# Optimization experiments

Measured on AMD Instinct MI355X. Metric: run time of the kernel, lower is better.

The kernel has to match this reference:

```python
import jax, jax.numpy as jnp
import numpy as np

B_GRAPHS = 32   # number of graphs in the batch (static)
HEADS = 8
EPS = 1e-8


def _layer_norm(x, g, b):
    mu = x.mean(-1, keepdims=True)
    var = x.var(-1, keepdims=True)
    return (x - mu) * jax.lax.rsqrt(var + 1e-5) * g + b


def setup_inputs() -> dict:
    key = jax.random.key(0)
    ks = jax.random.split(key, 16)
    N, C, d, M = 5120, 128, 16, 256
    E = N * 16
    f32 = jnp.float32
    sc_c = 1.0 / np.sqrt(C)
    inp = {
        'x': jax.random.normal(ks[0], (N, C), f32),
        'pe_re': jax.random.normal(ks[1], (N, d), f32),
        'pe_im': jax.random.normal(ks[2], (N, d), f32),
        'wq': jax.random.normal(ks[3], (C, C), f32) * sc_c,
        'bq': jnp.zeros((C,), f32),
        'wk': jax.random.normal(ks[4], (C, C), f32) * sc_c,
        'bk': jnp.zeros((C,), f32),
        'wv': jax.random.normal(ks[5], (C, C), f32) * sc_c,
        'bv': jnp.zeros((C,), f32),
        'wo': jax.random.normal(ks[6], (C, C), f32) * sc_c,
        'bo': jnp.zeros((C,), f32),
        'pe_w1': jax.random.normal(ks[7], (4 * d, 2 * d), f32) * (1.0 / np.sqrt(4 * d)),
        'pe_b1': jnp.zeros((2 * d,), f32),
        'pe_w2': jax.random.normal(ks[8], (2 * d, HEADS), f32) * (1.0 / np.sqrt(2 * d)),
        'pe_b2': jnp.zeros((HEADS,), f32),
        'mlp_w1': jax.random.normal(ks[9], (C, 2 * C), f32) * sc_c,
        'mlp_b1': jnp.zeros((2 * C,), f32),
        'mlp_w2': jax.random.normal(ks[10], (2 * C, C), f32) * (1.0 / np.sqrt(2 * C)),
        'mlp_b2': jnp.zeros((C,), f32),
        'ln2_g': jnp.ones((C,), f32),
        'ln2_b': jnp.zeros((C,), f32),
        'ln3_g': jnp.ones((C,), f32),
        'ln3_b': jnp.zeros((C,), f32),
        'batch': jnp.sort(jax.random.randint(ks[11], (N,), 0, B_GRAPHS, jnp.int32)),
        'edge_index': jax.random.randint(ks[12], (2, E), 0, N, jnp.int32),
        'nmax': M,
    }
    return inp


def reference(x, pe_re, pe_im, wq, bq, wk, bk, wv, bv, wo, bo,
              pe_w1, pe_b1, pe_w2, pe_b2, mlp_w1, mlp_b1, mlp_w2, mlp_b2,
              ln2_g, ln2_b, ln3_g, ln3_b, batch, edge_index, nmax):
    N, C = x.shape
    H = HEADS
    dh = C // H
    M = nmax

    # --- to_dense_batch: ragged [N,*] -> dense [B, M, *] + mask ---
    counts = jax.ops.segment_sum(jnp.ones((N,), jnp.int32), batch, num_segments=B_GRAPHS)
    offsets = jnp.concatenate([jnp.zeros((1,), jnp.int32), jnp.cumsum(counts)[:-1]])
    intra = jnp.arange(N, dtype=jnp.int32) - offsets[batch]
    hd = jnp.zeros((B_GRAPHS, M, C), x.dtype).at[batch, intra].set(x)
    ar = jnp.zeros((B_GRAPHS, M, pe_re.shape[1]), x.dtype).at[batch, intra].set(pe_re)
    ai = jnp.zeros((B_GRAPHS, M, pe_im.shape[1]), x.dtype).at[batch, intra].set(pe_im)
    mask = jnp.zeros((B_GRAPHS, M), bool).at[batch, intra].set(True)

    # --- pairwise complex-angle PE bias ---
    pn = jnp.sqrt(ar * ar + ai * ai + EPS)                 # [B,M,d] complex_norm
    denom = pn[:, :, None, :] * pn[:, None, :, :] + EPS    # [B,M,M,d]
    # z_i * conj(z_j) normalized -> cos/sin of pairwise angle
    real = (ar[:, :, None, :] * ar[:, None, :, :] + ai[:, :, None, :] * ai[:, None, :, :]) / denom
    imag = (ai[:, :, None, :] * ar[:, None, :, :] - ar[:, :, None, :] * ai[:, None, :, :]) / denom
    pni = jnp.broadcast_to(pn[:, :, None, :], real.shape)
    pnj = jnp.broadcast_to(pn[:, None, :, :], real.shape)
    bias_in = jnp.concatenate([pni, pnj, real, imag], axis=-1)       # [B,M,M,4d]
    hb = jax.nn.relu(bias_in @ pe_w1 + pe_b1) @ pe_w2 + pe_b2        # [B,M,M,H]
    # torch: bias.transpose(1,-1) swaps dims 1 and 3 -> [B,H,M,M]
    bias = jnp.transpose(hb, (0, 3, 2, 1))                           # [B,H,q,k]

    # --- multi-head attention with float bias + key padding mask ---
    q = (hd @ wq + bq).reshape(B_GRAPHS, M, H, dh)
    k = (hd @ wk + bk).reshape(B_GRAPHS, M, H, dh)
    v = (hd @ wv + bv).reshape(B_GRAPHS, M, H, dh)
    scores = jnp.einsum('bihd,bjhd->bhij', q, k) / np.sqrt(dh) + bias
    scores = jnp.where(mask[:, None, None, :], scores, -1e9)
    attn = jax.nn.softmax(scores, axis=-1)
    o = jnp.einsum('bhij,bjhd->bihd', attn, v).reshape(B_GRAPHS, M, C)
    o = o @ wo + bo

    # --- back to ragged, residual, norms, FFN ---
    h = o[batch, intra] + x
    h = _layer_norm(h, ln2_g, ln2_b)
    out = h + (jax.nn.relu(h @ mlp_w1 + mlp_b1) @ mlp_w2 + mlp_b2)
    out = _layer_norm(out, ln3_g, ln3_b)
    return out
```

## Files before the change

kernel.cpp:

```cpp
#include <hip/hip_runtime.h>

#define N_NODES 5120
#define C_DIM   128
#define D_PE    16
#define M_MAX   256
#define B_G     32
#define H_HEADS 8
#define DH      16
#define EPS_PE  1e-8f
#define QT      4
#define SCP     264

#define WS_COUNTS   0
#define WS_OFFSETS  32
#define WS_INTRA    64
#define WS_MASK     5184
#define WS_HD       13376
#define WS_AR       1061952
#define WS_AI       1193024
#define WS_PN       1324096
#define WS_CN       1455168
#define WS_KFHI     1717312
#define WS_KFLO     1979456
#define WS_Q        2110528
#define WS_K        3159104
#define WS_V        4207680
#define WS_OATT     5256256
#define WS_OPROJ    6304832
#define WS_HLN      7353408
#define WS_FFNH     8008768
#define WS_FFNO     9319488
#define WS_BIAS     9974848
#define WS_WPK_HI   18363456
#define WS_WPK_LO   18428992
#define WS_ZERO_FLOATS 1324096

#define WOFF_Q   0
#define WOFF_K   16384
#define WOFF_V   32768
#define WOFF_O   49152
#define WOFF_W1  65536
#define WOFF_W2  98304

typedef __attribute__((ext_vector_type(8))) short bf8_t;
typedef __attribute__((ext_vector_type(4))) float f4_t;

__device__ inline short f2bf(float f) {
    union { float f; unsigned u; } v; v.f = f;
    unsigned r = (v.u + 0x7FFF + ((v.u >> 16) & 1)) >> 16;
    return (short)r;
}
__device__ inline float bf2f(short h) {
    union { unsigned u; float f; } v; v.u = ((unsigned)(unsigned short)h) << 16;
    return v.f;
}
__device__ inline unsigned pack2(short a, short b) {
    return (unsigned)(unsigned short)a | ((unsigned)(unsigned short)b << 16);
}
__device__ inline bf8_t bf8_from2(uint2 a, uint2 b) {
    bf8_t o;
    o[0]=(short)a.x; o[1]=(short)(a.x>>16); o[2]=(short)a.y; o[3]=(short)(a.y>>16);
    o[4]=(short)b.x; o[5]=(short)(b.x>>16); o[6]=(short)b.y; o[7]=(short)(b.y>>16);
    return o;
}

__global__ __launch_bounds__(256) void setup_kernel(
    const int* __restrict__ batch, int* __restrict__ offsets, int* __restrict__ intra)
{
    __shared__ int cnt[B_G];
    __shared__ int off[B_G];
    const int t = threadIdx.x;
    if (t < B_G) cnt[t] = 0;
    __syncthreads();
    for (int n = t; n < N_NODES; n += 256) atomicAdd(&cnt[batch[n]], 1);
    __syncthreads();
    if (t == 0) { int s = 0; for (int b = 0; b < B_G; ++b) { off[b] = s; s += cnt[b]; } }
    __syncthreads();
    if (t < B_G) offsets[t] = off[t];
    for (int n = t; n < N_NODES; n += 256) intra[n] = n - off[batch[n]];
}

__global__ __launch_bounds__(128) void scatter_kernel(
    const float* __restrict__ x, const float* __restrict__ pre, const float* __restrict__ pim,
    const int* __restrict__ batch, const int* __restrict__ intra,
    float* __restrict__ hd, float* __restrict__ ar, float* __restrict__ ai,
    int* __restrict__ mask)
{
    const int n = blockIdx.x, c = threadIdx.x;
    const int b = batch[n], m = intra[n];
    hd[((size_t)b * M_MAX + m) * C_DIM + c] = x[(size_t)n * C_DIM + c];
    if (c < D_PE) {
        ar[((size_t)b * M_MAX + m) * D_PE + c] = pre[(size_t)n * D_PE + c];
        ai[((size_t)b * M_MAX + m) * D_PE + c] = pim[(size_t)n * D_PE + c];
    }
    if (c == 0) mask[b * M_MAX + m] = 1;
}

__global__ __launch_bounds__(256) void prep_kernel(
    const float* __restrict__ ar, const float* __restrict__ ai,
    float* __restrict__ pn, float* __restrict__ cn,
    unsigned short* __restrict__ kf_hi, unsigned short* __restrict__ kf_lo)
{
    const int idx = blockIdx.x * 256 + threadIdx.x;
    const int cell = idx >> 4, dd = idx & 15;
    const float a = ar[idx], b = ai[idx];
    const float p = sqrtf(a * a + b * b + EPS_PE);
    const float inv = 1.f / p;
    const float cr = a * inv, ci = b * inv;
    pn[idx] = p;
    cn[(size_t)cell * 32 + dd]      = cr;
    cn[(size_t)cell * 32 + 16 + dd] = ci;
    const size_t hb = (size_t)cell * 64, lb = (size_t)cell * 32;
    short crh = f2bf(cr), cih = f2bf(ci);
    kf_hi[hb + dd]      = (unsigned short)crh;
    kf_hi[hb + 16 + dd] = (unsigned short)cih;
    kf_hi[hb + 32 + dd] = (unsigned short)f2bf(p);
    kf_hi[hb + 48 + dd] = (dd == 0) ? (unsigned short)f2bf(1.f) : 0;
    kf_lo[lb + dd]      = (unsigned short)f2bf(cr - bf2f(crh));
    kf_lo[lb + 16 + dd] = (unsigned short)f2bf(ci - bf2f(cih));
}

__global__ __launch_bounds__(256) void wpack_kernel(
    const float* __restrict__ wq, const float* __restrict__ wk,
    const float* __restrict__ wv, const float* __restrict__ wo,
    const float* __restrict__ w1, const float* __restrict__ w2,
    unsigned short* __restrict__ hi, unsigned short* __restrict__ lo)
{
    const int tid = blockIdx.x * 256 + threadIdx.x;
    const int tile = tid >> 6, lane = tid & 63;
    const float* W; int N, ltile; size_t off;
    if (tile < 128) {
        const int wi = tile >> 5; ltile = tile & 31; N = 128;
        W = (wi == 0) ? wq : (wi == 1) ? wk : (wi == 2) ? wv : wo;
        off = (size_t)wi * 16384;
    } else if (tile < 192) { ltile = tile - 128; N = 256; W = w1; off = WOFF_W1; }
    else                   { ltile = tile - 192; N = 128; W = w2; off = WOFF_W2; }
    const int NT = N / 16;
    const int kt = ltile / NT, nt = ltile % NT;
    const int col = nt * 16 + (lane & 15);
    const int k0  = kt * 32 + (lane >> 4) * 8;
    bf8_t vhi, vlo;
    #pragma unroll
    for (int e = 0; e < 8; ++e) {
        const float v = W[(size_t)(k0 + e) * N + col];
        const short h = f2bf(v);
        vhi[e] = h; vlo[e] = f2bf(v - bf2f(h));
    }
    const size_t toff = off + ((size_t)ltile * 64 + lane) * 8;
    *(bf8_t*)(hi + toff) = vhi;
    *(bf8_t*)(lo + toff) = vlo;
}

template<int K, int N, bool RELU, bool RES>
__device__ inline void mgemm_body(
    const float* __restrict__ A, const unsigned short* __restrict__ hi,
    const unsigned short* __restrict__ lo,
    const float* __restrict__ bias, const float* __restrict__ res,
    float* __restrict__ out, int bx)
{
    constexpr int NT = N / 16, KT = K / 32;
    const int rb = bx * 64;
    const int w = threadIdx.x >> 6, lane = threadIdx.x & 63;
    const int arow = rb + w * 16 + (lane & 15);
    const int g = lane >> 4;

    f4_t acc[NT];
    #pragma unroll
    for (int nt = 0; nt < NT; ++nt) acc[nt] = (f4_t){0.f, 0.f, 0.f, 0.f};

    #pragma unroll
    for (int kt = 0; kt < KT; ++kt) {
        const float* ap = A + (size_t)arow * K + kt * 32 + g * 8;
        const float4 a0 = *(const float4*)ap;
        const float4 a1 = *(const float4*)(ap + 4);
        const float av[8] = {a0.x, a0.y, a0.z, a0.w, a1.x, a1.y, a1.z, a1.w};
        bf8_t ahi, alo;
        #pragma unroll
        for (int e = 0; e < 8; ++e) {
            const short h = f2bf(av[e]);
            ahi[e] = h; alo[e] = f2bf(av[e] - bf2f(h));
        }
        #pragma unroll
        for (int nt = 0; nt < NT; ++nt) {
            const size_t toff = ((size_t)(kt * NT + nt) * 64 + lane) * 8;
            const bf8_t bhi = *(const bf8_t*)(hi + toff);
            const bf8_t blo = *(const bf8_t*)(lo + toff);
            acc[nt] = __builtin_amdgcn_mfma_f32_16x16x32_bf16(ahi, bhi, acc[nt], 0, 0, 0);
            acc[nt] = __builtin_amdgcn_mfma_f32_16x16x32_bf16(alo, bhi, acc[nt], 0, 0, 0);
            acc[nt] = __builtin_amdgcn_mfma_f32_16x16x32_bf16(ahi, blo, acc[nt], 0, 0, 0);
        }
    }

    const int orow0 = rb + w * 16 + g * 4;
    #pragma unroll
    for (int nt = 0; nt < NT; ++nt) {
        const int col = nt * 16 + (lane & 15);
        const float bv = bias[col];
        #pragma unroll
        for (int r = 0; r < 4; ++r) {
            float v = acc[nt][r] + bv;
            if (RELU) v = fmaxf(v, 0.f);
            if (RES)  v += res[(size_t)(orow0 + r) * N + col];
            out[(size_t)(orow0 + r) * N + col] = v;
        }
    }
}

__global__ __launch_bounds__(256) void qkv_kernel(
    const float* __restrict__ A,
    const unsigned short* __restrict__ hi, const unsigned short* __restrict__ lo,
    const float* __restrict__ bq, const float* __restrict__ bk, const float* __restrict__ bv,
    float* __restrict__ qm, float* __restrict__ km, float* __restrict__ vm)
{
    const int sel = blockIdx.y;
    const float* bias = (sel == 0) ? bq : (sel == 1) ? bk : bv;
    float* out = (sel == 0) ? qm : (sel == 1) ? km : vm;
    const size_t woff = (size_t)sel * 16384;
    mgemm_body<128, 128, false, false>(A, hi + woff, lo + woff, bias, nullptr, out, blockIdx.x);
}

template<int K, int N, bool RELU, bool RES>
__global__ __launch_bounds__(256) void mgemm_kernel(
    const float* __restrict__ A,
    const unsigned short* __restrict__ hi, const unsigned short* __restrict__ lo,
    const float* __restrict__ bias, const float* __restrict__ res, float* __restrict__ out)
{
    mgemm_body<K, N, RELU, RES>(A, hi, lo, bias, res, out, blockIdx.x);
}

__global__ __launch_bounds__(512) void bias_kernel(
    const float* __restrict__ cn, const float* __restrict__ pn,
    const unsigned short* __restrict__ kf_hi, const unsigned short* __restrict__ kf_lo,
    const float* __restrict__ w1, const float* __restrict__ b1,
    const float* __restrict__ w2, const float* __restrict__ b2,
    unsigned short* __restrict__ bias_out)
{
    __shared__ float sW1T[32][65];
    __shared__ float s_cn[16][32];
    __shared__ float s_pn[16][16];
    __shared__ uint2 s_scr[8][16][10];

    const int b  = blockIdx.y;
    const int i0 = blockIdx.x * 16;
    const int t  = threadIdx.x;

    for (int idx = t; idx < 2048; idx += 512) {
        int f = idx >> 5, hh = idx & 31;
        sW1T[hh][f] = w1[f * 32 + hh];
    }
    { int il = t >> 5, c = t & 31;
      s_cn[il][c] = cn[((size_t)(b * 256 + i0 + il)) * 32 + c]; }
    if (t < 256) { int il = t >> 4, dd = t & 15;
      s_pn[il][dd] = pn[((size_t)(b * 256 + i0 + il)) * 16 + dd]; }
    __syncthreads();

    const int w    = t >> 6;
    const int lane = t & 63;
    const int lj   = lane & 15;
    const int g    = lane >> 4;

    bf8_t a2f;
    #pragma unroll
    for (int e = 0; e < 8; ++e) {
        float v = (lj < 8) ? w2[(g * 8 + e) * 8 + lj] : 0.f;
        a2f[e] = f2bf(v);
    }
    float b2v0 = 0.f, b2v1 = 0.f, b2v2 = 0.f, b2v3 = 0.f;
    if (g < 2) { b2v0 = b2[g*4+0]; b2v1 = b2[g*4+1]; b2v2 = b2[g*4+2]; b2v3 = b2[g*4+3]; }

    for (int ii = 0; ii < 2; ++ii) {
        const int il = w * 2 + ii;
        const int i  = i0 + il;

        float vrow0 = b1[lj], vrow1 = b1[16 + lj];
        #pragma unroll
        for (int dd = 0; dd < 16; ++dd) {
            float p = s_pn[il][dd];
            vrow0 = fmaf(sW1T[lj][16 + dd],      p, vrow0);
            vrow1 = fmaf(sW1T[16 + lj][16 + dd], p, vrow1);
        }

        bf8_t a0hi0, a0lo0, a1f0, a0hi1, a0lo1, a1f1;
        #pragma unroll
        for (int e = 0; e < 8; ++e) {
            const int dd = (g & 1) * 8 + e;
            const float cr = s_cn[il][dd], ci = s_cn[il][16 + dd];
            {
                float wr = sW1T[lj][32 + dd], wi = sW1T[lj][48 + dd];
                float val = (g < 2) ? (wr * cr - wi * ci) : (wr * ci + wi * cr);
                short hi = f2bf(val);
                a0hi0[e] = hi; a0lo0[e] = f2bf(val - bf2f(hi));
                float v1 = (g < 2) ? sW1T[lj][g * 8 + e]
                                   : ((g == 2 && e == 0) ? vrow0 : 0.f);
                a1f0[e] = f2bf(v1);
            }
            {
                float wr = sW1T[16 + lj][32 + dd], wi = sW1T[16 + lj][48 + dd];
                float val = (g < 2) ? (wr * cr - wi * ci) : (wr * ci + wi * cr);
                short hi = f2bf(val);
                a0hi1[e] = hi; a0lo1[e] = f2bf(val - bf2f(hi));
                float v1 = (g < 2) ? sW1T[16 + lj][g * 8 + e]
                                   : ((g == 2 && e == 0) ? vrow1 : 0.f);
                a1f1[e] = f2bf(v1);
            }
        }

        for (int jt = 0; jt < 16; ++jt) {
            const size_t node = (size_t)b * 256 + jt * 16 + lj;
            const bf8_t* ph = (const bf8_t*)(kf_hi + node * 64);
            const bf8_t* pl = (const bf8_t*)(kf_lo + node * 32);
            bf8_t b0hi = ph[g];
            bf8_t b0lo = pl[g];
            bf8_t b1f  = ph[4 + g];

            f4_t acc0 = {0.f, 0.f, 0.f, 0.f}, acc1 = {0.f, 0.f, 0.f, 0.f};
            acc0 = __builtin_amdgcn_mfma_f32_16x16x32_bf16(a0hi0, b0hi, acc0, 0, 0, 0);
            acc0 = __builtin_amdgcn_mfma_f32_16x16x32_bf16(a0hi0, b0lo, acc0, 0, 0, 0);
            acc0 = __builtin_amdgcn_mfma_f32_16x16x32_bf16(a0lo0, b0hi, acc0, 0, 0, 0);
            acc0 = __builtin_amdgcn_mfma_f32_16x16x32_bf16(a1f0,  b1f,  acc0, 0, 0, 0);
            acc1 = __builtin_amdgcn_mfma_f32_16x16x32_bf16(a0hi1, b0hi, acc1, 0, 0, 0);
            acc1 = __builtin_amdgcn_mfma_f32_16x16x32_bf16(a0hi1, b0lo, acc1, 0, 0, 0);
            acc1 = __builtin_amdgcn_mfma_f32_16x16x32_bf16(a0lo1, b0hi, acc1, 0, 0, 0);
            acc1 = __builtin_amdgcn_mfma_f32_16x16x32_bf16(a1f1,  b1f,  acc1, 0, 0, 0);

            uint2 w0, w1p;
            w0.x  = pack2(f2bf(fmaxf(acc0[0], 0.f)), f2bf(fmaxf(acc0[1], 0.f)));
            w0.y  = pack2(f2bf(fmaxf(acc0[2], 0.f)), f2bf(fmaxf(acc0[3], 0.f)));
            w1p.x = pack2(f2bf(fmaxf(acc1[0], 0.f)), f2bf(fmaxf(acc1[1], 0.f)));
            w1p.y = pack2(f2bf(fmaxf(acc1[2], 0.f)), f2bf(fmaxf(acc1[3], 0.f)));
            s_scr[w][lj][g]     = w0;
            s_scr[w][lj][4 + g] = w1p;
            __builtin_amdgcn_s_waitcnt(0);

            uint2 q0 = s_scr[w][lj][2 * g];
            uint2 q1 = s_scr[w][lj][2 * g + 1];
            bf8_t hb = bf8_from2(q0, q1);

            f4_t acc2 = {0.f, 0.f, 0.f, 0.f};
            acc2 = __builtin_amdgcn_mfma_f32_16x16x32_bf16(a2f, hb, acc2, 0, 0, 0);

            if (g < 2) {
                uint2 st;
                st.x = pack2(f2bf(acc2[0] + b2v0), f2bf(acc2[1] + b2v1));
                st.y = pack2(f2bf(acc2[2] + b2v2), f2bf(acc2[3] + b2v3));
                size_t idx = (((size_t)b * 256 + i) * 256 + jt * 16 + lj) * 8 + g * 4;
                *(uint2*)(bias_out + idx) = st;
            }
        }
    }
}

__global__ __launch_bounds__(256) void attn_kernel(
    const float* __restrict__ qm, const float* __restrict__ km, const float* __restrict__ vm,
    const int* __restrict__ mask, const unsigned short* __restrict__ bias,
    float* __restrict__ o_att)
{
    const int b  = blockIdx.y;
    const int i0 = blockIdx.x * QT;
    const int t  = threadIdx.x;
    const int j  = t;

    __shared__ float s_q[QT][C_DIM];
    __shared__ float s_sc[QT][H_HEADS][SCP];

    for (int idx = t; idx < QT * C_DIM; idx += 256) {
        const int qi = idx >> 7, c = idx & 127;
        s_q[qi][c] = qm[((size_t)(b * 256 + i0 + qi)) * C_DIM + c];
    }
    __syncthreads();

    const int mj = mask[b * M_MAX + j];
    uint4 bu[QT];
    #pragma unroll
    for (int qi = 0; qi < QT; ++qi)
        bu[qi] = *(const uint4*)(bias + (((size_t)(b * 256 + i0 + qi)) * 256 + j) * 8);

    const float* krow = km + ((size_t)(b * 256 + j)) * C_DIM;
    #pragma unroll
    for (int h = 0; h < 8; ++h) {
        float kv[DH];
        #pragma unroll
        for (int q4 = 0; q4 < 4; ++q4) {
            float4 v = ((const float4*)(krow + h * DH))[q4];
            kv[q4*4+0]=v.x; kv[q4*4+1]=v.y; kv[q4*4+2]=v.z; kv[q4*4+3]=v.w;
        }
        #pragma unroll
        for (int qi = 0; qi < QT; ++qi) {
            float dot = 0.f;
            #pragma unroll
            for (int dd = 0; dd < DH; ++dd)
                dot = fmaf(s_q[qi][h * DH + dd], kv[dd], dot);
            const unsigned u = ((const unsigned*)&bu[qi])[h >> 1];
            const float bv = bf2f((short)((h & 1) ? (u >> 16) : (u & 0xffff)));
            s_sc[qi][h][j] = mj ? fmaf(dot, 0.25f, bv) : -1e9f;
        }
    }
    __syncthreads();

    {
        const int wave = t >> 6, lane = t & 63;
        for (int r = wave; r < QT * H_HEADS; r += 4) {
            float* row = ((float*)s_sc) + r * SCP;
            float x0 = row[lane], x1 = row[lane + 64], x2 = row[lane + 128], x3 = row[lane + 192];
            float mx = fmaxf(fmaxf(x0, x1), fmaxf(x2, x3));
            #pragma unroll
            for (int off = 32; off > 0; off >>= 1) mx = fmaxf(mx, __shfl_xor(mx, off, 64));
            float e0 = expf(x0 - mx), e1 = expf(x1 - mx), e2 = expf(x2 - mx), e3 = expf(x3 - mx);
            float s = e0 + e1 + e2 + e3;
            #pragma unroll
            for (int off = 32; off > 0; off >>= 1) s += __shfl_xor(s, off, 64);
            const float inv = 1.f / s;
            row[lane] = e0 * inv; row[lane + 64] = e1 * inv;
            row[lane + 128] = e2 * inv; row[lane + 192] = e3 * inv;
        }
    }
    __syncthreads();

    {
        const int c = t & 127;
        const int gq = t >> 7;
        const int h = c >> 4;
        const int qA = gq * 2, qB = gq * 2 + 1;
        const float* vb = vm + (size_t)b * M_MAX * C_DIM + c;
        float a0 = 0.f, a1 = 0.f;
        for (int jj = 0; jj < M_MAX; jj += 4) {
            float4 pA = *(const float4*)&s_sc[qA][h][jj];
            float4 pB = *(const float4*)&s_sc[qB][h][jj];
            float v0 = vb[(size_t)(jj + 0) * C_DIM];
            float v1 = vb[(size_t)(jj + 1) * C_DIM];
            float v2 = vb[(size_t)(jj + 2) * C_DIM];
            float v3 = vb[(size_t)(jj + 3) * C_DIM];
            a0 = fmaf(pA.x, v0, a0); a0 = fmaf(pA.y, v1, a0);
            a0 = fmaf(pA.z, v2, a0); a0 = fmaf(pA.w, v3, a0);
            a1 = fmaf(pB.x, v0, a1); a1 = fmaf(pB.y, v1, a1);
            a1 = fmaf(pB.z, v2, a1); a1 = fmaf(pB.w, v3, a1);
        }
        o_att[((size_t)(b * 256 + i0 + qA)) * C_DIM + c] = a0;
        o_att[((size_t)(b * 256 + i0 + qB)) * C_DIM + c] = a1;
    }
}

__global__ __launch_bounds__(128) void gather_res_ln_kernel(
    const float* __restrict__ op, const float* __restrict__ x,
    const int* __restrict__ batch, const int* __restrict__ intra,
    const float* __restrict__ g, const float* __restrict__ be, float* __restrict__ out)
{
    const int n = blockIdx.x, c = threadIdx.x;
    const int b = batch[n], m = intra[n];
    const float v = op[((size_t)b * M_MAX + m) * C_DIM + c] + x[(size_t)n * C_DIM + c];
    float s = v, sq = v * v;
    #pragma unroll
    for (int off = 32; off > 0; off >>= 1) {
        s  += __shfl_xor(s, off, 64);
        sq += __shfl_xor(sq, off, 64);
    }
    __shared__ float red[4];
    if ((threadIdx.x & 63) == 0) {
        red[(threadIdx.x >> 6) * 2]     = s;
        red[(threadIdx.x >> 6) * 2 + 1] = sq;
    }
    __syncthreads();
    s = red[0] + red[2]; sq = red[1] + red[3];
    const float mu  = s * (1.f / C_DIM);
    const float var = sq * (1.f / C_DIM) - mu * mu;
    const float sc  = rsqrtf(var + 1e-5f);
    out[(size_t)n * C_DIM + c] = (v - mu) * sc * g[c] + be[c];
}

__global__ __launch_bounds__(128) void ln_kernel(
    const float* __restrict__ in, const float* __restrict__ g,
    const float* __restrict__ be, float* __restrict__ out)
{
    const int n = blockIdx.x, c = threadIdx.x;
    const float v = in[(size_t)n * C_DIM + c];
    float s = v, sq = v * v;
    #pragma unroll
    for (int off = 32; off > 0; off >>= 1) {
        s  += __shfl_xor(s, off, 64);
        sq += __shfl_xor(sq, off, 64);
    }
    __shared__ float red[4];
    if ((threadIdx.x & 63) == 0) {
        red[(threadIdx.x >> 6) * 2]     = s;
        red[(threadIdx.x >> 6) * 2 + 1] = sq;
    }
    __syncthreads();
    s = red[0] + red[2]; sq = red[1] + red[3];
    const float mu  = s * (1.f / C_DIM);
    const float var = sq * (1.f / C_DIM) - mu * mu;
    const float sc  = rsqrtf(var + 1e-5f);
    out[(size_t)n * C_DIM + c] = (v - mu) * sc * g[c] + be[c];
}

extern "C" void kernel_launch(void* const* d_in, const int* in_sizes, int n_in,
                              void* d_out, int out_size, void* d_ws, size_t ws_size,
                              hipStream_t stream)
{
    const float* x      = (const float*)d_in[0];
    const float* pe_re  = (const float*)d_in[1];
    const float* pe_im  = (const float*)d_in[2];
    const float* wq     = (const float*)d_in[3];
    const float* bq     = (const float*)d_in[4];
    const float* wk     = (const float*)d_in[5];
    const float* bk     = (const float*)d_in[6];
    const float* wv     = (const float*)d_in[7];
    const float* bv     = (const float*)d_in[8];
    const float* wo     = (const float*)d_in[9];
    const float* bo     = (const float*)d_in[10];
    const float* pe_w1  = (const float*)d_in[11];
    const float* pe_b1  = (const float*)d_in[12];
    const float* pe_w2  = (const float*)d_in[13];
    const float* pe_b2  = (const float*)d_in[14];
    const float* mlp_w1 = (const float*)d_in[15];
    const float* mlp_b1 = (const float*)d_in[16];
    const float* mlp_w2 = (const float*)d_in[17];
    const float* mlp_b2 = (const float*)d_in[18];
    const float* ln2_g  = (const float*)d_in[19];
    const float* ln2_b  = (const float*)d_in[20];
    const float* ln3_g  = (const float*)d_in[21];
    const float* ln3_b  = (const float*)d_in[22];
    const int*   batch  = (const int*)d_in[23];

    float* ws = (float*)d_ws;
    int*   offsets = (int*)(ws + WS_OFFSETS);
    int*   intra   = (int*)(ws + WS_INTRA);
    int*   mask    = (int*)(ws + WS_MASK);
    float* hd   = ws + WS_HD;
    float* ar   = ws + WS_AR;
    float* ai   = ws + WS_AI;
    float* pn   = ws + WS_PN;
    float* cn   = ws + WS_CN;
    unsigned short* kf_hi = (unsigned short*)(ws + WS_KFHI);
    unsigned short* kf_lo = (unsigned short*)(ws + WS_KFLO);
    float* qm   = ws + WS_Q;
    float* km   = ws + WS_K;
    float* vm   = ws + WS_V;
    float* oatt = ws + WS_OATT;
    float* oprj = ws + WS_OPROJ;
    float* hln  = ws + WS_HLN;
    float* ffnh = ws + WS_FFNH;
    float* ffno = ws + WS_FFNO;
    unsigned short* bias = (unsigned short*)(ws + WS_BIAS);
    unsigned short* wpk_hi = (unsigned short*)(ws + WS_WPK_HI);
    unsigned short* wpk_lo = (unsigned short*)(ws + WS_WPK_LO);
    float* outp = (float*)d_out;

    hipMemsetAsync(d_ws, 0, (size_t)WS_ZERO_FLOATS * sizeof(float), stream);

    setup_kernel<<<1, 256, 0, stream>>>(batch, offsets, intra);
    wpack_kernel<<<64, 256, 0, stream>>>(wq, wk, wv, wo, mlp_w1, mlp_w2, wpk_hi, wpk_lo);
    scatter_kernel<<<N_NODES, 128, 0, stream>>>(x, pe_re, pe_im, batch, intra, hd, ar, ai, mask);
    prep_kernel<<<512, 256, 0, stream>>>(ar, ai, pn, cn, kf_hi, kf_lo);

    qkv_kernel<<<dim3(128, 3), 256, 0, stream>>>(hd, wpk_hi, wpk_lo, bq, bk, bv, qm, km, vm);

    bias_kernel<<<dim3(16, 32), 512, 0, stream>>>(cn, pn, kf_hi, kf_lo,
                                                  pe_w1, pe_b1, pe_w2, pe_b2, bias);

    attn_kernel<<<dim3(M_MAX / QT, B_G), 256, 0, stream>>>(qm, km, vm, mask, bias, oatt);

    mgemm_kernel<128, 128, false, false><<<128, 256, 0, stream>>>(
        oatt, wpk_hi + WOFF_O, wpk_lo + WOFF_O, bo, nullptr, oprj);
    gather_res_ln_kernel<<<N_NODES, 128, 0, stream>>>(oprj, x, batch, intra, ln2_g, ln2_b, hln);
    mgemm_kernel<128, 256, true, false><<<80, 256, 0, stream>>>(
        hln, wpk_hi + WOFF_W1, wpk_lo + WOFF_W1, mlp_b1, nullptr, ffnh);
    mgemm_kernel<256, 128, false, true><<<80, 256, 0, stream>>>(
        ffnh, wpk_hi + WOFF_W2, wpk_lo + WOFF_W2, mlp_b2, hln, ffno);
    ln_kernel<<<N_NODES, 128, 0, stream>>>(ffno, ln3_g, ln3_b, outp);
}
```

Before: 315.1 us.

## Fuse scatter into QKV/prep, fuse GEMM with residual+LayerNorm, skip padded rows

Result: slower. 325.1 us (+3.2%).

```diff
diff --git a/kernel.cpp b/kernel.cpp
--- a/kernel.cpp
+++ b/kernel.cpp
@@ -8,36 +8,28 @@
 #define H_HEADS 8
 #define DH      16
 #define EPS_PE  1e-8f
-#define QT      4
+#define QT      2
 #define SCP     264
 
 #define WS_COUNTS   0
 #define WS_OFFSETS  32
 #define WS_INTRA    64
 #define WS_MASK     5184
-#define WS_HD       13376
-#define WS_AR       1061952
-#define WS_AI       1193024
-#define WS_PN       1324096
-#define WS_CN       1455168
-#define WS_KFHI     1717312
-#define WS_KFLO     1979456
-#define WS_Q        2110528
-#define WS_K        3159104
-#define WS_V        4207680
-#define WS_OATT     5256256
-#define WS_OPROJ    6304832
-#define WS_HLN      7353408
-#define WS_FFNH     8008768
-#define WS_FFNO     9319488
-#define WS_BIAS     9974848
-#define WS_WPK_HI   18363456
-#define WS_WPK_LO   18428992
-#define WS_ZERO_FLOATS 1324096
-
-#define WOFF_Q   0
-#define WOFF_K   16384
-#define WOFF_V   32768
+#define WS_CN       13376
+#define WS_PN       275520
+#define WS_KFHI     406592
+#define WS_KFLO     668736
+#define WS_QM       799808
+#define WS_KM       1848384
+#define WS_VM       2896960
+#define WS_OATT     3945536
+#define WS_HLN      4994112
+#define WS_FFNH     5649472
+#define WS_BIAS     6960192
+#define WS_WPK_HI   15348800
+#define WS_WPK_LO   15414336
+#define WS_ZERO_FLOATS 13376
+
 #define WOFF_O   49152
 #define WOFF_W1  65536
 #define WOFF_W2  98304
@@ -65,7 +57,8 @@
 }
 
 __global__ __launch_bounds__(256) void setup_kernel(
-    const int* __restrict__ batch, int* __restrict__ offsets, int* __restrict__ intra)
+    const int* __restrict__ batch, int* __restrict__ counts_o,
+    int* __restrict__ offsets, int* __restrict__ intra)
 {
     __shared__ int cnt[B_G];
     __shared__ int off[B_G];
@@ -76,41 +69,29 @@
     __syncthreads();
     if (t == 0) { int s = 0; for (int b = 0; b < B_G; ++b) { off[b] = s; s += cnt[b]; } }
     __syncthreads();
-    if (t < B_G) offsets[t] = off[t];
+    if (t < B_G) { offsets[t] = off[t]; counts_o[t] = cnt[t]; }
     for (int n = t; n < N_NODES; n += 256) intra[n] = n - off[batch[n]];
 }
 
-__global__ __launch_bounds__(128) void scatter_kernel(
-    const float* __restrict__ x, const float* __restrict__ pre, const float* __restrict__ pim,
+__global__ __launch_bounds__(256) void prep_kernel(
+    const float* __restrict__ pre, const float* __restrict__ pim,
     const int* __restrict__ batch, const int* __restrict__ intra,
-    float* __restrict__ hd, float* __restrict__ ar, float* __restrict__ ai,
+    float* __restrict__ pn, float* __restrict__ cn,
+    unsigned short* __restrict__ kf_hi, unsigned short* __restrict__ kf_lo,
     int* __restrict__ mask)
 {
-    const int n = blockIdx.x, c = threadIdx.x;
+    const int idx = blockIdx.x * 256 + threadIdx.x;
+    const int n = idx >> 4, dd = idx & 15;
     const int b = batch[n], m = intra[n];
-    hd[((size_t)b * M_MAX + m) * C_DIM + c] = x[(size_t)n * C_DIM + c];
-    if (c < D_PE) {
-        ar[((size_t)b * M_MAX + m) * D_PE + c] = pre[(size_t)n * D_PE + c];
-        ai[((size_t)b * M_MAX + m) * D_PE + c] = pim[(size_t)n * D_PE + c];
-    }
-    if (c == 0) mask[b * M_MAX + m] = 1;
-}
-
-__global__ __launch_bounds__(256) void prep_kernel(
-    const float* __restrict__ ar, const float* __restrict__ ai,
-    float* __restrict__ pn, float* __restrict__ cn,
-    unsigned short* __restrict__ kf_hi, unsigned short* __restrict__ kf_lo)
-{
-    const int idx = blockIdx.x * 256 + threadIdx.x;
-    const int cell = idx >> 4, dd = idx & 15;
-    const float a = ar[idx], b = ai[idx];
-    const float p = sqrtf(a * a + b * b + EPS_PE);
+    const size_t cell = (size_t)b * M_MAX + m;
+    const float a = pre[(size_t)n * D_PE + dd], bb = pim[(size_t)n * D_PE + dd];
+    const float p = sqrtf(a * a + bb * bb + EPS_PE);
     const float inv = 1.f / p;
-    const float cr = a * inv, ci = b * inv;
-    pn[idx] = p;
-    cn[(size_t)cell * 32 + dd]      = cr;
-    cn[(size_t)cell * 32 + 16 + dd] = ci;
-    const size_t hb = (size_t)cell * 64, lb = (size_t)cell * 32;
+    const float cr = a * inv, ci = bb * inv;
+    pn[cell * 16 + dd] = p;
+    cn[cell * 32 + dd]      = cr;
+    cn[cell * 32 + 16 + dd] = ci;
+    const size_t hb = cell * 64, lb = cell * 32;
     short crh = f2bf(cr), cih = f2bf(ci);
     kf_hi[hb + dd]      = (unsigned short)crh;
     kf_hi[hb + 16 + dd] = (unsigned short)cih;
@@ -118,6 +99,7 @@
     kf_hi[hb + 48 + dd] = (dd == 0) ? (unsigned short)f2bf(1.f) : 0;
     kf_lo[lb + dd]      = (unsigned short)f2bf(cr - bf2f(crh));
     kf_lo[lb + 16 + dd] = (unsigned short)f2bf(ci - bf2f(cih));
+    if (dd == 0) mask[cell] = 1;
 }
 
 __global__ __launch_bounds__(256) void wpack_kernel(
@@ -151,26 +133,17 @@
     *(bf8_t*)(lo + toff) = vlo;
 }
 
-template<int K, int N, bool RELU, bool RES>
-__device__ inline void mgemm_body(
-    const float* __restrict__ A, const unsigned short* __restrict__ hi,
-    const unsigned short* __restrict__ lo,
-    const float* __restrict__ bias, const float* __restrict__ res,
-    float* __restrict__ out, int bx)
+template<int K, int N>
+__device__ inline void mgemm_core(
+    const float* __restrict__ Arow,
+    const unsigned short* __restrict__ hi, const unsigned short* __restrict__ lo,
+    int lane, f4_t* acc)
 {
     constexpr int NT = N / 16, KT = K / 32;
-    const int rb = bx * 64;
-    const int w = threadIdx.x >> 6, lane = threadIdx.x & 63;
-    const int arow = rb + w * 16 + (lane & 15);
     const int g = lane >> 4;
-
-    f4_t acc[NT];
-    #pragma unroll
-    for (int nt = 0; nt < NT; ++nt) acc[nt] = (f4_t){0.f, 0.f, 0.f, 0.f};
-
     #pragma unroll
     for (int kt = 0; kt < KT; ++kt) {
-        const float* ap = A + (size_t)arow * K + kt * 32 + g * 8;
+        const float* ap = Arow + kt * 32 + g * 8;
         const float4 a0 = *(const float4*)ap;
         const float4 a1 = *(const float4*)(ap + 4);
         const float av[8] = {a0.x, a0.y, a0.z, a0.w, a1.x, a1.y, a1.z, a1.w};
@@ -190,42 +163,136 @@
             acc[nt] = __builtin_amdgcn_mfma_f32_16x16x32_bf16(ahi, blo, acc[nt], 0, 0, 0);
         }
     }
+}
+
+__global__ __launch_bounds__(256) void qkv_node_kernel(
+    const float* __restrict__ x,
+    const unsigned short* __restrict__ hi, const unsigned short* __restrict__ lo,
+    const float* __restrict__ bq, const float* __restrict__ bk, const float* __restrict__ bv,
+    const int* __restrict__ batch, const int* __restrict__ intra,
+    float* __restrict__ qm, float* __restrict__ km, float* __restrict__ vm)
+{
+    const int sel = blockIdx.y;
+    const float* bias = (sel == 0) ? bq : (sel == 1) ? bk : bv;
+    float* out = (sel == 0) ? qm : (sel == 1) ? km : vm;
+    const unsigned short* whi = hi + (size_t)sel * 16384;
+    const unsigned short* wlo = lo + (size_t)sel * 16384;
+
+    const int rb = blockIdx.x * 64;
+    const int w = threadIdx.x >> 6, lane = threadIdx.x & 63;
+    const int lj = lane & 15, g = lane >> 4;
+    const int arow = rb + w * 16 + lj;
+
+    f4_t acc[8];
+    #pragma unroll
+    for (int nt = 0; nt < 8; ++nt) acc[nt] = (f4_t){0.f, 0.f, 0.f, 0.f};
+    mgemm_core<128, 128>(x + (size_t)arow * 128, whi, wlo, lane, acc);
 
     const int orow0 = rb + w * 16 + g * 4;
+    int dst[4];
+    #pragma unroll
+    for (int r = 0; r < 4; ++r) {
+        const int nr = orow0 + r;
+        dst[r] = batch[nr] * M_MAX + intra[nr];
+    }
+    #pragma unroll
+    for (int nt = 0; nt < 8; ++nt) {
+        const int col = nt * 16 + lj;
+        const float bv_ = bias[col];
+        #pragma unroll
+        for (int r = 0; r < 4; ++r)
+            out[(size_t)dst[r] * 128 + col] = acc[nt][r] + bv_;
+    }
+}
+
+template<int K, int N, bool RELU>
+__global__ __launch_bounds__(256) void mgemm_kernel(
+    const float* __restrict__ A,
+    const unsigned short* __restrict__ hi, const unsigned short* __restrict__ lo,
+    const float* __restrict__ bias, float* __restrict__ out)
+{
+    constexpr int NT = N / 16;
+    const int rb = blockIdx.x * 64;
+    const int w = threadIdx.x >> 6, lane = threadIdx.x & 63;
+    const int lj = lane & 15, g = lane >> 4;
+    const int arow = rb + w * 16 + lj;
+
+    f4_t acc[NT];
+    #pragma unroll
+    for (int nt = 0; nt < NT; ++nt) acc[nt] = (f4_t){0.f, 0.f, 0.f, 0.f};
+    mgemm_core<K, N>(A + (size_t)arow * K, hi, lo, lane, acc);
+
+    const int orow0 = rb + w * 16 + g * 4;
     #pragma unroll
     for (int nt = 0; nt < NT; ++nt) {
-        const int col = nt * 16 + (lane & 15);
+        const int col = nt * 16 + lj;
         const float bv = bias[col];
         #pragma unroll
         for (int r = 0; r < 4; ++r) {
             float v = acc[nt][r] + bv;
             if (RELU) v = fmaxf(v, 0.f);
-            if (RES)  v += res[(size_t)(orow0 + r) * N + col];
             out[(size_t)(orow0 + r) * N + col] = v;
         }
     }
 }
 
-__global__ __launch_bounds__(256) void qkv_kernel(
+template<int K, bool GATHER_A>
+__global__ __launch_bounds__(256) void gemm_res_ln_kernel(
     const float* __restrict__ A,
     const unsigned short* __restrict__ hi, const unsigned short* __restrict__ lo,
-    const float* __restrict__ bq, const float* __restrict__ bk, const float* __restrict__ bv,
-    float* __restrict__ qm, float* __restrict__ km, float* __restrict__ vm)
-{
-    const int sel = blockIdx.y;
-    const float* bias = (sel == 0) ? bq : (sel == 1) ? bk : bv;
-    float* out = (sel == 0) ? qm : (sel == 1) ? km : vm;
-    const size_t woff = (size_t)sel * 16384;
-    mgemm_body<128, 128, false, false>(A, hi + woff, lo + woff, bias, nullptr, out, blockIdx.x);
-}
-
-template<int K, int N, bool RELU, bool RES>
-__global__ __launch_bounds__(256) void mgemm_kernel(
-    const float* __restrict__ A,
-    const unsigned short* __restrict__ hi, const unsigned short* __restrict__ lo,
-    const float* __restrict__ bias, const float* __restrict__ res, float* __restrict__ out)
-{
-    mgemm_body<K, N, RELU, RES>(A, hi, lo, bias, res, out, blockIdx.x);
+    const float* __restrict__ bias, const float* __restrict__ res,
+    const int* __restrict__ batch, const int* __restrict__ intra,
+    const float* __restrict__ lng, const float* __restrict__ lnb,
+    float* __restrict__ out)
+{
+    __shared__ float sOut[64][133];
+    __shared__ float red_s[64][4];
+    __shared__ float red_q[64][4];
+
+    const int rb = blockIdx.x * 64;
+    const int w = threadIdx.x >> 6, lane = threadIdx.x & 63;
+    const int lj = lane & 15, g = lane >> 4;
+    const int arow = rb + w * 16 + lj;
+    const size_t asrc = GATHER_A ? (size_t)(batch[arow] * M_MAX + intra[arow]) : (size_t)arow;
+
+    f4_t acc[8];
+    #pragma unroll
+    for (int nt = 0; nt < 8; ++nt) acc[nt] = (f4_t){0.f, 0.f, 0.f, 0.f};
+    mgemm_core<K, 128>(A + asrc * K, hi, lo, lane, acc);
+
+    const int lrow0 = w * 16 + g * 4;
+    #pragma unroll
+    for (int nt = 0; nt < 8; ++nt) {
+        const int col = nt * 16 + lj;
+        const float bv = bias[col];
+        #pragma unroll
+        for (int r = 0; r < 4; ++r)
+            sOut[lrow0 + r][col] = acc[nt][r] + bv;
+    }
+    __syncthreads();
+
+    const int row = threadIdx.x >> 2, seg = threadIdx.x & 3;
+    const int n = rb + row;
+    float s = 0.f, sq = 0.f;
+    #pragma unroll
+    for (int i = 0; i < 32; ++i) {
+        const int c = 4 * i + seg;
+        const float v = sOut[row][c] + res[(size_t)n * 128 + c];
+        sOut[row][c] = v;
+        s += v; sq += v * v;
+    }
+    red_s[row][seg] = s; red_q[row][seg] = sq;
+    __syncthreads();
+    s  = red_s[row][0] + red_s[row][1] + red_s[row][2] + red_s[row][3];
+    sq = red_q[row][0] + red_q[row][1] + red_q[row][2] + red_q[row][3];
+    const float mu  = s * (1.f / 128.f);
+    const float var = sq * (1.f / 128.f) - mu * mu;
+    const float sc  = rsqrtf(var + 1e-5f);
+    #pragma unroll
+    for (int i = 0; i < 32; ++i) {
+        const int c = 4 * i + seg;
+        out[(size_t)n * 128 + c] = (sOut[row][c] - mu) * sc * lng[c] + lnb[c];
+    }
 }
 
 __global__ __launch_bounds__(512) void bias_kernel(
@@ -233,15 +300,18 @@
     const unsigned short* __restrict__ kf_hi, const unsigned short* __restrict__ kf_lo,
     const float* __restrict__ w1, const float* __restrict__ b1,
     const float* __restrict__ w2, const float* __restrict__ b2,
+    const int* __restrict__ counts,
     unsigned short* __restrict__ bias_out)
 {
+    const int b  = blockIdx.y;
+    const int i0 = blockIdx.x * 16;
+    if (i0 >= counts[b]) return;
+
     __shared__ float sW1T[32][65];
     __shared__ float s_cn[16][32];
     __shared__ float s_pn[16][16];
     __shared__ uint2 s_scr[8][16][10];
 
-    const int b  = blockIdx.y;
-    const int i0 = blockIdx.x * 16;
     const int t  = threadIdx.x;
 
     for (int idx = t; idx < 2048; idx += 512) {
@@ -353,18 +423,20 @@
 __global__ __launch_bounds__(256) void attn_kernel(
     const float* __restrict__ qm, const float* __restrict__ km, const float* __restrict__ vm,
     const int* __restrict__ mask, const unsigned short* __restrict__ bias,
+    const int* __restrict__ counts,
     float* __restrict__ o_att)
 {
     const int b  = blockIdx.y;
     const int i0 = blockIdx.x * QT;
+    if (i0 >= counts[b]) return;
     const int t  = threadIdx.x;
     const int j  = t;
 
     __shared__ float s_q[QT][C_DIM];
     __shared__ float s_sc[QT][H_HEADS][SCP];
 
-    for (int idx = t; idx < QT * C_DIM; idx += 256) {
-        const int qi = idx >> 7, c = idx & 127;
+    {
+        const int qi = t >> 7, c = t & 127;
         s_q[qi][c] = qm[((size_t)(b * 256 + i0 + qi)) * C_DIM + c];
     }
     __syncthreads();
@@ -420,76 +492,17 @@
         const int c = t & 127;
         const int gq = t >> 7;
         const int h = c >> 4;
-        const int qA = gq * 2, qB = gq * 2 + 1;
         const float* vb = vm + (size_t)b * M_MAX * C_DIM + c;
-        float a0 = 0.f, a1 = 0.f;
+        float a0 = 0.f;
         for (int jj = 0; jj < M_MAX; jj += 4) {
-            float4 pA = *(const float4*)&s_sc[qA][h][jj];
-            float4 pB = *(const float4*)&s_sc[qB][h][jj];
-            float v0 = vb[(size_t)(jj + 0) * C_DIM];
-            float v1 = vb[(size_t)(jj + 1) * C_DIM];
-            float v2 = vb[(size_t)(jj + 2) * C_DIM];
-            float v3 = vb[(size_t)(jj + 3) * C_DIM];
-            a0 = fmaf(pA.x, v0, a0); a0 = fmaf(pA.y, v1, a0);
-            a0 = fmaf(pA.z, v2, a0); a0 = fmaf(pA.w, v3, a0);
-            a1 = fmaf(pB.x, v0, a1); a1 = fmaf(pB.y, v1, a1);
-            a1 = fmaf(pB.z, v2, a1); a1 = fmaf(pB.w, v3, a1);
-        }
-        o_att[((size_t)(b * 256 + i0 + qA)) * C_DIM + c] = a0;
-        o_att[((size_t)(b * 256 + i0 + qB)) * C_DIM + c] = a1;
-    }
-}
-
-__global__ __launch_bounds__(128) void gather_res_ln_kernel(
-    const float* __restrict__ op, const float* __restrict__ x,
-    const int* __restrict__ batch, const int* __restrict__ intra,
-    const float* __restrict__ g, const float* __restrict__ be, float* __restrict__ out)
-{
-    const int n = blockIdx.x, c = threadIdx.x;
-    const int b = batch[n], m = intra[n];
-    const float v = op[((size_t)b * M_MAX + m) * C_DIM + c] + x[(size_t)n * C_DIM + c];
-    float s = v, sq = v * v;
-    #pragma unroll
-    for (int off = 32; off > 0; off >>= 1) {
-        s  += __shfl_xor(s, off, 64);
-        sq += __shfl_xor(sq, off, 64);
-    }
-    __shared__ float red[4];
-    if ((threadIdx.x & 63) == 0) {
-        red[(threadIdx.x >> 6) * 2]     = s;
-        red[(threadIdx.x >> 6) * 2 + 1] = sq;
-    }
-    __syncthreads();
-    s = red[0] + red[2]; sq = red[1] + red[3];
-    const float mu  = s * (1.f / C_DIM);
-    const float var = sq * (1.f / C_DIM) - mu * mu;
-    const float sc  = rsqrtf(var + 1e-5f);
-    out[(size_t)n * C_DIM + c] = (v - mu) * sc * g[c] + be[c];
-}
-
-__global__ __launch_bounds__(128) void ln_kernel(
-    const float* __restrict__ in, const float* __restrict__ g,
-    const float* __restrict__ be, float* __restrict__ out)
-{
-    const int n = blockIdx.x, c = threadIdx.x;
-    const float v = in[(size_t)n * C_DIM + c];
-    float s = v, sq = v * v;
-    #pragma unroll
-    for (int off = 32; off > 0; off >>= 1) {
-        s  += __shfl_xor(s, off, 64);
-        sq += __shfl_xor(sq, off, 64);
-    }
-    __shared__ float red[4];
-    if ((threadIdx.x & 63) == 0) {
-        red[(threadIdx.x >> 6) * 2]     = s;
-        red[(threadIdx.x >> 6) * 2 + 1] = sq;
-    }
-    __syncthreads();
-    s = red[0] + red[2]; sq = red[1] + red[3];
-    const float mu  = s * (1.f / C_DIM);
-    const float var = sq * (1.f / C_DIM) - mu * mu;
-    const float sc  = rsqrtf(var + 1e-5f);
-    out[(size_t)n * C_DIM + c] = (v - mu) * sc * g[c] + be[c];
+            float4 pA = *(const float4*)&s_sc[gq][h][jj];
+            a0 = fmaf(pA.x, vb[(size_t)(jj + 0) * C_DIM], a0);
+            a0 = fmaf(pA.y, vb[(size_t)(jj + 1) * C_DIM], a0);
+            a0 = fmaf(pA.z, vb[(size_t)(jj + 2) * C_DIM], a0);
+            a0 = fmaf(pA.w, vb[(size_t)(jj + 3) * C_DIM], a0);
+        }
+        o_att[((size_t)(b * 256 + i0 + gq)) * C_DIM + c] = a0;
+    }
 }
 
 extern "C" void kernel_launch(void* const* d_in, const int* in_sizes, int n_in,
@@ -522,24 +535,20 @@
     const int*   batch  = (const int*)d_in[23];
 
     float* ws = (float*)d_ws;
+    int*   counts  = (int*)(ws + WS_COUNTS);
     int*   offsets = (int*)(ws + WS_OFFSETS);
     int*   intra   = (int*)(ws + WS_INTRA);
     int*   mask    = (int*)(ws + WS_MASK);
-    float* hd   = ws + WS_HD;
-    float* ar   = ws + WS_AR;
-    float* ai   = ws + WS_AI;
+    float* cn   = ws + WS_CN;
     float* pn   = ws + WS_PN;
-    float* cn   = ws + WS_CN;
     unsigned short* kf_hi = (unsigned short*)(ws + WS_KFHI);
     unsigned short* kf_lo = (unsigned short*)(ws + WS_KFLO);
-    float* qm   = ws + WS_Q;
-    float* km   = ws + WS_K;
-    float* vm   = ws + WS_V;
+    float* qm   = ws + WS_QM;
+    float* km   = ws + WS_KM;
+    float* vm   = ws + WS_VM;
     float* oatt = ws + WS_OATT;
-    float* oprj = ws + WS_OPROJ;
     float* hln  = ws + WS_HLN;
     float* ffnh = ws + WS_FFNH;
-    float* ffno = ws + WS_FFNO;
     unsigned short* bias = (unsigned short*)(ws + WS_BIAS);
     unsigned short* wpk_hi = (unsigned short*)(ws + WS_WPK_HI);
     unsigned short* wpk_lo = (unsigned short*)(ws + WS_WPK_LO);
@@ -547,24 +556,24 @@
 
     hipMemsetAsync(d_ws, 0, (size_t)WS_ZERO_FLOATS * sizeof(float), stream);
 
-    setup_kernel<<<1, 256, 0, stream>>>(batch, offsets, intra);
+    setup_kernel<<<1, 256, 0, stream>>>(batch, counts, offsets, intra);
     wpack_kernel<<<64, 256, 0, stream>>>(wq, wk, wv, wo, mlp_w1, mlp_w2, wpk_hi, wpk_lo);
-    scatter_kernel<<<N_NODES, 128, 0, stream>>>(x, pe_re, pe_im, batch, intra, hd, ar, ai, mask);
-    prep_kernel<<<512, 256, 0, stream>>>(ar, ai, pn, cn, kf_hi, kf_lo);
-
-    qkv_kernel<<<dim3(128, 3), 256, 0, stream>>>(hd, wpk_hi, wpk_lo, bq, bk, bv, qm, km, vm);
+    prep_kernel<<<320, 256, 0, stream>>>(pe_re, pe_im, batch, intra, pn, cn, kf_hi, kf_lo, mask);
+
+    qkv_node_kernel<<<dim3(80, 3), 256, 0, stream>>>(x, wpk_hi, wpk_lo, bq, bk, bv,
+                                                     batch, intra, qm, km, vm);
 
     bias_kernel<<<dim3(16, 32), 512, 0, stream>>>(cn, pn, kf_hi, kf_lo,
-                                                  pe_w1, pe_b1, pe_w2, pe_b2, bias);
-
-    attn_kernel<<<dim3(M_MAX / QT, B_G), 256, 0, stream>>>(qm, km, vm, mask, bias, oatt);
-
-    mgemm_kernel<128, 128, false, false><<<128, 256, 0, stream>>>(
-        oatt, wpk_hi + WOFF_O, wpk_lo + WOFF_O, bo, nullptr, oprj);
-    gather_res_ln_kernel<<<N_NODES, 128, 0, stream>>>(oprj, x, batch, intra, ln2_g, ln2_b, hln);
-    mgemm_kernel<128, 256, true, false><<<80, 256, 0, stream>>>(
-        hln, wpk_hi + WOFF_W1, wpk_lo + WOFF_W1, mlp_b1, nullptr, ffnh);
-    mgemm_kernel<256, 128, false, true><<<80, 256, 0, stream>>>(
-        ffnh, wpk_hi + WOFF_W2, wpk_lo + WOFF_W2, mlp_b2, hln, ffno);
-    ln_kernel<<<N_NODES, 128, 0, stream>>>(ffno, ln3_g, ln3_b, outp);
-}
+                                                  pe_w1, pe_b1, pe_w2, pe_b2, counts, bias);
+
+    attn_kernel<<<dim3(M_MAX / QT, B_G), 256, 0, stream>>>(qm, km, vm, mask, bias, counts, oatt);
+
+    gemm_res_ln_kernel<128, true><<<80, 256, 0, stream>>>(
+        oatt, wpk_hi + WOFF_O, wpk_lo + WOFF_O, bo, x, batch, intra, ln2_g, ln2_b, hln);
+
+    mgemm_kernel<128, 256, true><<<80, 256, 0, stream>>>(
+        hln, wpk_hi + WOFF_W1, wpk_lo + WOFF_W1, mlp_b1, ffnh);
+
+    gemm_res_ln_kernel<256, false><<<80, 256, 0, stream>>>(
+        ffnh, wpk_hi + WOFF_W2, wpk_lo + WOFF_W2, mlp_b2, hln, batch, intra, ln3_g, ln3_b, outp);
+}
```
